# Kernel optimization log

Hardware: AMD Instinct MI355X
Metric: run time of the kernel (lower is better)

## Reference

```python
import jax, jax.numpy as jnp
import numpy as np

NUM_LAYERS = 3
CH = 8            # dynamic head channels
CIN = 8           # mask-branch feature channels
MASK_OUT_STRIDE = 4
WEIGHT_NUMS = [(CIN + 2) * CH, CH * CH, CH * 1]
BIAS_NUMS = [CH, CH, 1]
NUM_GEN_PARAMS = sum(WEIGHT_NUMS) + sum(BIAS_NUMS)  # 169


def compute_locations(h, w, stride):
    # FCOS-style pixel center locations, x-coordinate first: (H*W, 2)
    sx = jnp.arange(w, dtype=jnp.float32) * stride + stride // 2
    sy = jnp.arange(h, dtype=jnp.float32) * stride + stride // 2
    yy, xx = jnp.meshgrid(sy, sx, indexing='ij')
    return jnp.stack([xx.reshape(-1), yy.reshape(-1)], axis=1)


def _resize_axis_align_corners(x, factor, axis):
    # Bilinear, align_corners=True, out_size = factor*(in_size-1)+1.
    # Source coords are exactly j/factor, so interpolation weights are static.
    s = x.shape[axis] - 1
    j = jnp.arange(factor * s + 1)
    i0 = j // factor
    i1 = jnp.minimum(i0 + 1, s)
    frac = (j % factor).astype(x.dtype) / factor
    shp = [1] * x.ndim
    shp[axis] = -1
    frac = frac.reshape(shp)
    return jnp.take(x, i0, axis=axis) * (1 - frac) + jnp.take(x, i1, axis=axis) * frac


def aligned_bilinear(t, factor):
    if factor == 1:
        return t
    h, w = t.shape[2], t.shape[3]
    t = jnp.pad(t, ((0, 0), (0, 0), (0, 1), (0, 1)), mode='edge')   # replicate pad bottom/right
    t = _resize_axis_align_corners(t, factor, 2)                     # -> factor*h + 1
    t = _resize_axis_align_corners(t, factor, 3)                     # -> factor*w + 1
    p = factor // 2
    t = jnp.pad(t, ((0, 0), (0, 0), (p, 0), (p, 0)), mode='edge')    # replicate pad top/left
    return t[:, :, :factor * h, :factor * w]


def parse_params(params):
    # params: (n_inst, 169) -> per-instance weights/biases of the 3 1x1 conv layers
    n = params.shape[0]
    idx = np.cumsum(WEIGHT_NUMS + BIAS_NUMS)[:-1]
    w0, w1, w2, b0, b1, b2 = jnp.split(params, idx, axis=1)
    w0 = w0.reshape(n, CH, CIN + 2)
    w1 = w1.reshape(n, CH, CH)
    w2 = w2.reshape(n, 1, CH)
    b2 = b2.reshape(n, 1)
    return (w0, w1, w2), (b0, b1, b2)


def dynamic_mask_head(mask_feats, mask_head_params, locations, im_inds, fpn_levels, sizes_of_interest, mask_feat_stride):
    N, C, H, W = mask_feats.shape
    n_inst = mask_head_params.shape[0]
    locs = compute_locations(H, W, mask_feat_stride)                 # (HW, 2)
    rel = locations[:, None, :] - locs[None, :, :]                   # (n, HW, 2)
    rel = jnp.transpose(rel, (0, 2, 1))                              # (n, 2, HW)
    soi = sizes_of_interest[fpn_levels]                              # (n,)
    rel = (rel / soi[:, None, None]).astype(mask_feats.dtype)
    feats = mask_feats[im_inds].reshape(n_inst, CIN, H * W)          # gather per-instance image feats
    x = jnp.concatenate([rel, feats], axis=1)                        # (n, CIN+2, HW)
    (w0, w1, w2), (b0, b1, b2) = parse_params(mask_head_params)
    # grouped 1x1 convs (groups = n_inst) == per-instance small matmuls
    x = jax.nn.relu(jnp.einsum('noi,nip->nop', w0, x) + b0[:, :, None])
    x = jax.nn.relu(jnp.einsum('noi,nip->nop', w1, x) + b1[:, :, None])
    x = jnp.einsum('noi,nip->nop', w2, x) + b2[:, :, None]           # (n, 1, HW)
    logits = x.reshape(n_inst, 1, H, W)
    logits = aligned_bilinear(logits, mask_feat_stride // MASK_OUT_STRIDE)
    return jax.nn.sigmoid(logits)


def setup_inputs() -> dict:
    key = jax.random.key(0)
    k1, k2, k3, k4, k5 = jax.random.split(key, 5)
    N, H, W, n_inst = 2, 136, 200, 128
    mask_feats = jax.random.normal(k1, (N, CIN, H, W), dtype=jnp.float32)
    mask_head_params = jax.random.normal(k2, (n_inst, NUM_GEN_PARAMS), dtype=jnp.float32) * 0.1
    locations = jax.random.uniform(k3, (n_inst, 2), dtype=jnp.float32) * 1600.0
    im_inds = jax.random.randint(k4, (n_inst,), 0, N)
    fpn_levels = jax.random.randint(k5, (n_inst,), 0, 5)
    sizes_of_interest = jnp.array([64.0, 128.0, 256.0, 512.0, 1024.0], dtype=jnp.float32)
    return {"mask_feats": mask_feats, "mask_head_params": mask_head_params, "locations": locations,
            "im_inds": im_inds, "fpn_levels": fpn_levels, "sizes_of_interest": sizes_of_interest,
            "mask_feat_stride": 8}


def reference(mask_feats, mask_head_params, locations, im_inds, fpn_levels, sizes_of_interest, mask_feat_stride):
    return dynamic_mask_head(mask_feats, mask_head_params, locations, im_inds, fpn_levels,
                             sizes_of_interest, mask_feat_stride)
```

## Files before the change

### kernel.cpp

```cpp
#include <hip/hip_runtime.h>
#include <math.h>

typedef __fp16 h2 __attribute__((ext_vector_type(2)));
typedef float  f4 __attribute__((ext_vector_type(4)));

#define H_IN   136
#define W_IN   200
#define HWP    (H_IN * W_IN)
#define OH     272
#define OW     400
#define RB     8
#define NSTRIP 17
#define LROWS  (RB + 1)
#define CH     8
#define CIN    8
#define NPARAM 169
#define NEG_LOG2E (-1.4426950408889634f)


__device__ __forceinline__ h2 pkrtz(float a, float b) {
    return __builtin_amdgcn_cvt_pkrtz(a, b);
}

__device__ __forceinline__ void nt_store4(float* p, float4 v) {
    f4 nv = {v.x, v.y, v.z, v.w};
    __builtin_nontemporal_store(nv, (f4*)p);
}

__global__ __launch_bounds__(256, 3) void mask_head_fused(
    const float* __restrict__ mask_feats,
    const float* __restrict__ params,
    const float* __restrict__ locations,
    const int*   __restrict__ im_inds,
    const int*   __restrict__ fpn_levels,
    const float* __restrict__ soi_tab,
    float* __restrict__ out)
{
    __shared__ h2    sW[NPARAM];
    __shared__ float T[LROWS][W_IN];

    const int inst = blockIdx.y;
    const int r0   = blockIdx.x * RB;
    const int tid  = threadIdx.x;

    const float* F = mask_feats + (size_t)im_inds[inst] * (CIN * HWP);

    const int  k_u = tid / 25;
    const int  c_u = (tid - k_u * 25) * 8;
    const int  r_u = min(max(r0 - 1 + k_u, 0), H_IN - 1);
    const bool p1  = (tid < LROWS * 25);

    float4 fA[CIN], fB[CIN];
    if (p1) {
        #pragma unroll
        for (int ch = 0; ch < CIN; ++ch) {
            const float* q = F + ch * HWP + r_u * W_IN + c_u;
            fA[ch] = *(const float4*)q;
            fB[ch] = *(const float4*)(q + 4);
        }
    }

    const float* P = params + inst * NPARAM;
    if (tid < NPARAM) {
        float w = P[tid];
        if ((tid >= 144 && tid < 152) || tid == 168) w *= NEG_LOG2E;
        const __fp16 hw = (__fp16)w;
        h2 v; v.x = hw; v.y = hw;
        sW[tid] = v;
    }

    const float loc_x   = locations[2 * inst];
    const float loc_y   = locations[2 * inst + 1];
    const float inv_soi = 1.0f / soi_tab[fpn_levels[inst]];
    float* O = out + (size_t)inst * (OH * OW);
    __syncthreads();

    if (p1) {
        h2 f[CIN][4];
        #pragma unroll
        for (int ch = 0; ch < CIN; ++ch) {
            f[ch][0] = pkrtz(fA[ch].x, fA[ch].y); f[ch][1] = pkrtz(fA[ch].z, fA[ch].w);
            f[ch][2] = pkrtz(fB[ch].x, fB[ch].y); f[ch][3] = pkrtz(fB[ch].z, fB[ch].w);
        }

        const float ry  = (loc_y - (float)(r_u * 8 + 4)) * inv_soi;
        const float dx  = -8.0f * inv_soi;
        const float rx0 = (loc_x - (float)(c_u * 8 + 4)) * inv_soi;
        h2 rxh[4];
        #pragma unroll
        for (int s = 0; s < 4; ++s)
            rxh[s] = pkrtz(rx0 + (float)(2 * s) * dx, rx0 + (float)(2 * s + 1) * dx);
        const h2 ryh = pkrtz(ry, ry);
        const h2 z2  = {(__fp16)0.0f, (__fp16)0.0f};

        h2 h0[CH][4];
        #pragma unroll
        for (int o = 0; o < CH; ++o) {
            const h2 base = __builtin_elementwise_fma(sW[o * 10 + 1], ryh, sW[152 + o]);
            const h2 wx = sW[o * 10];
            h2 a[4];
            #pragma unroll
            for (int s = 0; s < 4; ++s) a[s] = __builtin_elementwise_fma(wx, rxh[s], base);
            #pragma unroll
            for (int i = 0; i < CIN; ++i) {
                const h2 w = sW[o * 10 + 2 + i];
                #pragma unroll
                for (int s = 0; s < 4; ++s) a[s] = __builtin_elementwise_fma(w, f[i][s], a[s]);
            }
            #pragma unroll
            for (int s = 0; s < 4; ++s) h0[o][s] = __builtin_elementwise_max(a[s], z2);
        }

        h2 h1[CH][4];
        #pragma unroll
        for (int o = 0; o < CH; ++o) {
            const h2 b = sW[160 + o];
            h2 a[4] = {b, b, b, b};
            #pragma unroll
            for (int i = 0; i < CH; ++i) {
                const h2 w = sW[80 + o * CH + i];
                #pragma unroll
                for (int s = 0; s < 4; ++s) a[s] = __builtin_elementwise_fma(w, h0[i][s], a[s]);
            }
            #pragma unroll
            for (int s = 0; s < 4; ++s) h1[o][s] = __builtin_elementwise_max(a[s], z2);
        }

        const h2 b2 = sW[168];
        h2 t[4] = {b2, b2, b2, b2};
        #pragma unroll
        for (int i = 0; i < CH; ++i) {
            const h2 w = sW[144 + i];
            #pragma unroll
            for (int s = 0; s < 4; ++s) t[s] = __builtin_elementwise_fma(w, h1[i][s], t[s]);
        }

        *(float4*)&T[k_u][c_u] = make_float4((float)t[0].x, (float)t[0].y,
                                             (float)t[1].x, (float)t[1].y);
        *(float4*)&T[k_u][c_u + 4] = make_float4((float)t[2].x, (float)t[2].y,
                                                 (float)t[3].x, (float)t[3].y);
    }
    __syncthreads();

    #pragma unroll
    for (int it = 0; it < 2; ++it) {
        const int s = tid + 256 * it;
        if (s < RB * (W_IN / 4)) {
            const int rpl = s / (W_IN / 4);
            const int t   = s - rpl * (W_IN / 4);
            const int cm  = 4 * t;
            const int cl  = max(cm - 1, 0);

            const float4 mR = *(const float4*)&T[rpl + 1][cm];
            const float4 mQ = *(const float4*)&T[rpl][cm];
            const float  AR = T[rpl + 1][cl];
            const float  AQ = T[rpl][cl];

            const float Aa = 0.5f * (AR + AQ);
            const float Ba = 0.5f * (mR.x + mQ.x);
            const float Ca = 0.5f * (mR.y + mQ.y);
            const float Da = 0.5f * (mR.z + mQ.z);
            const float Ea = 0.5f * (mR.w + mQ.w);

            float4 s0, s1, s2, s3;
            s0.x = __builtin_amdgcn_rcpf(1.0f + __builtin_amdgcn_exp2f(0.5f * (Aa + Ba)));
            s0.y = __builtin_amdgcn_rcpf(1.0f + __builtin_amdgcn_exp2f(Ba));
            s0.z = __builtin_amdgcn_rcpf(1.0f + __builtin_amdgcn_exp2f(0.5f * (Ba + Ca)));
            s0.w = __builtin_amdgcn_rcpf(1.0f + __builtin_amdgcn_exp2f(Ca));
            s1.x = __builtin_amdgcn_rcpf(1.0f + __builtin_amdgcn_exp2f(0.5f * (Ca + Da)));
            s1.y = __builtin_amdgcn_rcpf(1.0f + __builtin_amdgcn_exp2f(Da));
            s1.z = __builtin_amdgcn_rcpf(1.0f + __builtin_amdgcn_exp2f(0.5f * (Da + Ea)));
            s1.w = __builtin_amdgcn_rcpf(1.0f + __builtin_amdgcn_exp2f(Ea));

            s2.x = __builtin_amdgcn_rcpf(1.0f + __builtin_amdgcn_exp2f(0.5f * (AR + mR.x)));
            s2.y = __builtin_amdgcn_rcpf(1.0f + __builtin_amdgcn_exp2f(mR.x));
            s2.z = __builtin_amdgcn_rcpf(1.0f + __builtin_amdgcn_exp2f(0.5f * (mR.x + mR.y)));
            s2.w = __builtin_amdgcn_rcpf(1.0f + __builtin_amdgcn_exp2f(mR.y));
            s3.x = __builtin_amdgcn_rcpf(1.0f + __builtin_amdgcn_exp2f(0.5f * (mR.y + mR.z)));
            s3.y = __builtin_amdgcn_rcpf(1.0f + __builtin_amdgcn_exp2f(mR.z));
            s3.z = __builtin_amdgcn_rcpf(1.0f + __builtin_amdgcn_exp2f(0.5f * (mR.z + mR.w)));
            s3.w = __builtin_amdgcn_rcpf(1.0f + __builtin_amdgcn_exp2f(mR.w));

            float* O0 = O + (size_t)(2 * (r0 + rpl)) * OW + 8 * t;
            nt_store4(O0,          s0);
            nt_store4(O0 + 4,      s1);
            nt_store4(O0 + OW,     s2);
            nt_store4(O0 + OW + 4, s3);
        }
    }
}

extern "C" void kernel_launch(void* const* d_in, const int* in_sizes, int n_in,
                              void* d_out, int out_size, void* d_ws, size_t ws_size,
                              hipStream_t stream) {
    const float* mask_feats = (const float*)d_in[0];
    const float* params     = (const float*)d_in[1];
    const float* locations  = (const float*)d_in[2];
    const int*   im_inds    = (const int*)d_in[3];
    const int*   fpn_levels = (const int*)d_in[4];
    const float* soi_tab    = (const float*)d_in[5];

    const int n_inst = in_sizes[1] / NPARAM;
    dim3 grid(NSTRIP, n_inst);
    mask_head_fused<<<grid, 256, 0, stream>>>(
        mask_feats, params, locations, im_inds, fpn_levels, soi_tab, (float*)d_out);
}
```

Before: 24.18 us.

## Split strip MLP into two phases overlapping upsample stores with second-half compute

Each thread now evaluates the per-pixel MLP on 4 pixels instead of 8. The 9 low-res rows are computed in two phases: rows 0-4 first, then rows 5-8, which are loaded and computed while the upper half of the output is upsampled and stored. This is meant to overlap global stores and transcendental work with MLP compute and cut register pressure. The cost is an extra barrier, fewer active threads (250 and 200 of 256) and more serialised phases per block.

New measurement: 24.69 us. 1.02x slower.

```diff
diff --git a/kernel.cpp b/kernel.cpp
--- a/kernel.cpp
+++ b/kernel.cpp
@@ -27,6 +27,109 @@
     __builtin_nontemporal_store(nv, (f4*)p);
 }
 
+__device__ __forceinline__ float4 mlp4h(const h2* sW, const float4* fv,
+                                        float loc_x, float loc_y, float inv_soi,
+                                        int r, int c)
+{
+    h2 f[CIN][2];
+    #pragma unroll
+    for (int ch = 0; ch < CIN; ++ch) {
+        f[ch][0] = pkrtz(fv[ch].x, fv[ch].y);
+        f[ch][1] = pkrtz(fv[ch].z, fv[ch].w);
+    }
+    const float ry  = (loc_y - (float)(r * 8 + 4)) * inv_soi;
+    const float dx  = -8.0f * inv_soi;
+    const float rx0 = (loc_x - (float)(c * 8 + 4)) * inv_soi;
+    h2 rxh[2];
+    rxh[0] = pkrtz(rx0, rx0 + dx);
+    rxh[1] = pkrtz(rx0 + 2.0f * dx, rx0 + 3.0f * dx);
+    const h2 ryh = pkrtz(ry, ry);
+    const h2 z2  = {(__fp16)0.0f, (__fp16)0.0f};
+
+    h2 h0[CH][2];
+    #pragma unroll
+    for (int o = 0; o < CH; ++o) {
+        const h2 base = __builtin_elementwise_fma(sW[o * 10 + 1], ryh, sW[152 + o]);
+        const h2 wx = sW[o * 10];
+        h2 a0 = __builtin_elementwise_fma(wx, rxh[0], base);
+        h2 a1 = __builtin_elementwise_fma(wx, rxh[1], base);
+        #pragma unroll
+        for (int i = 0; i < CIN; ++i) {
+            const h2 w = sW[o * 10 + 2 + i];
+            a0 = __builtin_elementwise_fma(w, f[i][0], a0);
+            a1 = __builtin_elementwise_fma(w, f[i][1], a1);
+        }
+        h0[o][0] = __builtin_elementwise_max(a0, z2);
+        h0[o][1] = __builtin_elementwise_max(a1, z2);
+    }
+    h2 h1[CH][2];
+    #pragma unroll
+    for (int o = 0; o < CH; ++o) {
+        const h2 b = sW[160 + o];
+        h2 a0 = b, a1 = b;
+        #pragma unroll
+        for (int i = 0; i < CH; ++i) {
+            const h2 w = sW[80 + o * CH + i];
+            a0 = __builtin_elementwise_fma(w, h0[i][0], a0);
+            a1 = __builtin_elementwise_fma(w, h0[i][1], a1);
+        }
+        h1[o][0] = __builtin_elementwise_max(a0, z2);
+        h1[o][1] = __builtin_elementwise_max(a1, z2);
+    }
+    const h2 b2 = sW[168];
+    h2 t0 = b2, t1 = b2;
+    #pragma unroll
+    for (int i = 0; i < CH; ++i) {
+        const h2 w = sW[144 + i];
+        t0 = __builtin_elementwise_fma(w, h1[i][0], t0);
+        t1 = __builtin_elementwise_fma(w, h1[i][1], t1);
+    }
+    return make_float4((float)t0.x, (float)t0.y, (float)t1.x, (float)t1.y);
+}
+
+__device__ __forceinline__ void upsample16(
+    const float (*T)[W_IN], float* __restrict__ O, int r0, int rpl, int t)
+{
+    const int cm = 4 * t;
+    const int cl = max(cm - 1, 0);
+
+    const float4 mR = *(const float4*)&T[rpl + 1][cm];
+    const float4 mQ = *(const float4*)&T[rpl][cm];
+    const float  AR = T[rpl + 1][cl];
+    const float  AQ = T[rpl][cl];
+
+    const float Aa = 0.5f * (AR + AQ);
+    const float Ba = 0.5f * (mR.x + mQ.x);
+    const float Ca = 0.5f * (mR.y + mQ.y);
+    const float Da = 0.5f * (mR.z + mQ.z);
+    const float Ea = 0.5f * (mR.w + mQ.w);
+
+    float4 s0, s1, s2, s3;
+    s0.x = __builtin_amdgcn_rcpf(1.0f + __builtin_amdgcn_exp2f(0.5f * (Aa + Ba)));
+    s0.y = __builtin_amdgcn_rcpf(1.0f + __builtin_amdgcn_exp2f(Ba));
+    s0.z = __builtin_amdgcn_rcpf(1.0f + __builtin_amdgcn_exp2f(0.5f * (Ba + Ca)));
+    s0.w = __builtin_amdgcn_rcpf(1.0f + __builtin_amdgcn_exp2f(Ca));
+    s1.x = __builtin_amdgcn_rcpf(1.0f + __builtin_amdgcn_exp2f(0.5f * (Ca + Da)));
+    s1.y = __builtin_amdgcn_rcpf(1.0f + __builtin_amdgcn_exp2f(Da));
+    s1.z = __builtin_amdgcn_rcpf(1.0f + __builtin_amdgcn_exp2f(0.5f * (Da + Ea)));
+    s1.w = __builtin_amdgcn_rcpf(1.0f + __builtin_amdgcn_exp2f(Ea));
+
+    s2.x = __builtin_amdgcn_rcpf(1.0f + __builtin_amdgcn_exp2f(0.5f * (AR + mR.x)));
+    s2.y = __builtin_amdgcn_rcpf(1.0f + __builtin_amdgcn_exp2f(mR.x));
+    s2.z = __builtin_amdgcn_rcpf(1.0f + __builtin_amdgcn_exp2f(0.5f * (mR.x + mR.y)));
+    s2.w = __builtin_amdgcn_rcpf(1.0f + __builtin_amdgcn_exp2f(mR.y));
+    s3.x = __builtin_amdgcn_rcpf(1.0f + __builtin_amdgcn_exp2f(0.5f * (mR.y + mR.z)));
+    s3.y = __builtin_amdgcn_rcpf(1.0f + __builtin_amdgcn_exp2f(mR.z));
+    s3.z = __builtin_amdgcn_rcpf(1.0f + __builtin_amdgcn_exp2f(0.5f * (mR.z + mR.w)));
+    s3.w = __builtin_amdgcn_rcpf(1.0f + __builtin_amdgcn_exp2f(mR.w));
+
+    float* O0 = O + (size_t)(2 * (r0 + rpl)) * OW + 8 * t;
+    nt_store4(O0,          s0);
+    nt_store4(O0 + 4,      s1);
+    nt_store4(O0 + OW,     s2);
+    nt_store4(O0 + OW + 4, s3);
+}
+
 __global__ __launch_bounds__(256, 3) void mask_head_fused(
     const float* __restrict__ mask_feats,
     const float* __restrict__ params,
@@ -45,19 +148,16 @@
 
     const float* F = mask_feats + (size_t)im_inds[inst] * (CIN * HWP);
 
-    const int  k_u = tid / 25;
-    const int  c_u = (tid - k_u * 25) * 8;
-    const int  r_u = min(max(r0 - 1 + k_u, 0), H_IN - 1);
-    const bool p1  = (tid < LROWS * 25);
-
-    float4 fA[CIN], fB[CIN];
-    if (p1) {
-        #pragma unroll
-        for (int ch = 0; ch < CIN; ++ch) {
-            const float* q = F + ch * HWP + r_u * W_IN + c_u;
-            fA[ch] = *(const float4*)q;
-            fB[ch] = *(const float4*)(q + 4);
-        }
+    const int  ka = tid / 50;
+    const int  ca = (tid - ka * 50) * 4;
+    const int  ra = min(max(r0 - 1 + ka, 0), H_IN - 1);
+    const bool p1a = (tid < 5 * 50);
+
+    float4 fa[CIN];
+    if (p1a) {
+        #pragma unroll
+        for (int ch = 0; ch < CIN; ++ch)
+            fa[ch] = *(const float4*)(F + ch * HWP + ra * W_IN + ca);
     }
 
     const float* P = params + inst * NPARAM;
@@ -75,119 +175,29 @@
     float* O = out + (size_t)inst * (OH * OW);
     __syncthreads();
 
-    if (p1) {
-        h2 f[CIN][4];
-        #pragma unroll
-        for (int ch = 0; ch < CIN; ++ch) {
-            f[ch][0] = pkrtz(fA[ch].x, fA[ch].y); f[ch][1] = pkrtz(fA[ch].z, fA[ch].w);
-            f[ch][2] = pkrtz(fB[ch].x, fB[ch].y); f[ch][3] = pkrtz(fB[ch].z, fB[ch].w);
-        }
-
-        const float ry  = (loc_y - (float)(r_u * 8 + 4)) * inv_soi;
-        const float dx  = -8.0f * inv_soi;
-        const float rx0 = (loc_x - (float)(c_u * 8 + 4)) * inv_soi;
-        h2 rxh[4];
-        #pragma unroll
-        for (int s = 0; s < 4; ++s)
-            rxh[s] = pkrtz(rx0 + (float)(2 * s) * dx, rx0 + (float)(2 * s + 1) * dx);
-        const h2 ryh = pkrtz(ry, ry);
-        const h2 z2  = {(__fp16)0.0f, (__fp16)0.0f};
-
-        h2 h0[CH][4];
-        #pragma unroll
-        for (int o = 0; o < CH; ++o) {
-            const h2 base = __builtin_elementwise_fma(sW[o * 10 + 1], ryh, sW[152 + o]);
-            const h2 wx = sW[o * 10];
-            h2 a[4];
-            #pragma unroll
-            for (int s = 0; s < 4; ++s) a[s] = __builtin_elementwise_fma(wx, rxh[s], base);
-            #pragma unroll
-            for (int i = 0; i < CIN; ++i) {
-                const h2 w = sW[o * 10 + 2 + i];
-                #pragma unroll
-                for (int s = 0; s < 4; ++s) a[s] = __builtin_elementwise_fma(w, f[i][s], a[s]);
-            }
-            #pragma unroll
-            for (int s = 0; s < 4; ++s) h0[o][s] = __builtin_elementwise_max(a[s], z2);
-        }
-
-        h2 h1[CH][4];
-        #pragma unroll
-        for (int o = 0; o < CH; ++o) {
-            const h2 b = sW[160 + o];
-            h2 a[4] = {b, b, b, b};
-            #pragma unroll
-            for (int i = 0; i < CH; ++i) {
-                const h2 w = sW[80 + o * CH + i];
-                #pragma unroll
-                for (int s = 0; s < 4; ++s) a[s] = __builtin_elementwise_fma(w, h0[i][s], a[s]);
-            }
-            #pragma unroll
-            for (int s = 0; s < 4; ++s) h1[o][s] = __builtin_elementwise_max(a[s], z2);
-        }
-
-        const h2 b2 = sW[168];
-        h2 t[4] = {b2, b2, b2, b2};
-        #pragma unroll
-        for (int i = 0; i < CH; ++i) {
-            const h2 w = sW[144 + i];
-            #pragma unroll
-            for (int s = 0; s < 4; ++s) t[s] = __builtin_elementwise_fma(w, h1[i][s], t[s]);
-        }
-
-        *(float4*)&T[k_u][c_u] = make_float4((float)t[0].x, (float)t[0].y,
-                                             (float)t[1].x, (float)t[1].y);
-        *(float4*)&T[k_u][c_u + 4] = make_float4((float)t[2].x, (float)t[2].y,
-                                                 (float)t[3].x, (float)t[3].y);
-    }
+    if (p1a)
+        *(float4*)&T[ka][ca] = mlp4h(sW, fa, loc_x, loc_y, inv_soi, ra, ca);
     __syncthreads();
 
-    #pragma unroll
-    for (int it = 0; it < 2; ++it) {
-        const int s = tid + 256 * it;
-        if (s < RB * (W_IN / 4)) {
-            const int rpl = s / (W_IN / 4);
-            const int t   = s - rpl * (W_IN / 4);
-            const int cm  = 4 * t;
-            const int cl  = max(cm - 1, 0);
-
-            const float4 mR = *(const float4*)&T[rpl + 1][cm];
-            const float4 mQ = *(const float4*)&T[rpl][cm];
-            const float  AR = T[rpl + 1][cl];
-            const float  AQ = T[rpl][cl];
-
-            const float Aa = 0.5f * (AR + AQ);
-            const float Ba = 0.5f * (mR.x + mQ.x);
-            const float Ca = 0.5f * (mR.y + mQ.y);
-            const float Da = 0.5f * (mR.z + mQ.z);
-            const float Ea = 0.5f * (mR.w + mQ.w);
-
-            float4 s0, s1, s2, s3;
-            s0.x = __builtin_amdgcn_rcpf(1.0f + __builtin_amdgcn_exp2f(0.5f * (Aa + Ba)));
-            s0.y = __builtin_amdgcn_rcpf(1.0f + __builtin_amdgcn_exp2f(Ba));
-            s0.z = __builtin_amdgcn_rcpf(1.0f + __builtin_amdgcn_exp2f(0.5f * (Ba + Ca)));
-            s0.w = __builtin_amdgcn_rcpf(1.0f + __builtin_amdgcn_exp2f(Ca));
-            s1.x = __builtin_amdgcn_rcpf(1.0f + __builtin_amdgcn_exp2f(0.5f * (Ca + Da)));
-            s1.y = __builtin_amdgcn_rcpf(1.0f + __builtin_amdgcn_exp2f(Da));
-            s1.z = __builtin_amdgcn_rcpf(1.0f + __builtin_amdgcn_exp2f(0.5f * (Da + Ea)));
-            s1.w = __builtin_amdgcn_rcpf(1.0f + __builtin_amdgcn_exp2f(Ea));
-
-            s2.x = __builtin_amdgcn_rcpf(1.0f + __builtin_amdgcn_exp2f(0.5f * (AR + mR.x)));
-            s2.y = __builtin_amdgcn_rcpf(1.0f + __builtin_amdgcn_exp2f(mR.x));
-            s2.z = __builtin_amdgcn_rcpf(1.0f + __builtin_amdgcn_exp2f(0.5f * (mR.x + mR.y)));
-            s2.w = __builtin_amdgcn_rcpf(1.0f + __builtin_amdgcn_exp2f(mR.y));
-            s3.x = __builtin_amdgcn_rcpf(1.0f + __builtin_amdgcn_exp2f(0.5f * (mR.y + mR.z)));
-            s3.y = __builtin_amdgcn_rcpf(1.0f + __builtin_amdgcn_exp2f(mR.z));
-            s3.z = __builtin_amdgcn_rcpf(1.0f + __builtin_amdgcn_exp2f(0.5f * (mR.z + mR.w)));
-            s3.w = __builtin_amdgcn_rcpf(1.0f + __builtin_amdgcn_exp2f(mR.w));
-
-            float* O0 = O + (size_t)(2 * (r0 + rpl)) * OW + 8 * t;
-            nt_store4(O0,          s0);
-            nt_store4(O0 + 4,      s1);
-            nt_store4(O0 + OW,     s2);
-            nt_store4(O0 + OW + 4, s3);
-        }
-    }
+    const bool pb = (tid < 200);
+    const int  kb = 5 + tid / 50;
+    const int  cb = (tid - (tid / 50) * 50) * 4;
+    const int  rb = min(r0 - 1 + kb, H_IN - 1);
+
+    float4 fb[CIN];
+    if (pb) {
+        #pragma unroll
+        for (int ch = 0; ch < CIN; ++ch)
+            fb[ch] = *(const float4*)(F + ch * HWP + rb * W_IN + cb);
+    }
+    if (pb)
+        upsample16(T, O, r0, tid / 50, tid % 50);
+    if (pb)
+        *(float4*)&T[kb][cb] = mlp4h(sW, fb, loc_x, loc_y, inv_soi, rb, cb);
+    __syncthreads();
+
+    if (pb)
+        upsample16(T, O, r0, 4 + tid / 50, tid % 50);
 }
 
 extern "C" void kernel_launch(void* const* d_in, const int* in_sizes, int n_in,
```
